# Performance work log

Measured on AMD Instinct MI355X. Metric: run time of the kernel, lower is better.

Reference implementation:

```python
import jax, jax.numpy as jnp
import numpy as np

HEAD_SIZE = 64
NUM_HEADS = 16
D_MODEL = HEAD_SIZE * NUM_HEADS  # 1024
B, S = 2, 2048


def setup_inputs() -> dict:
    key = jax.random.key(0)
    ks = jax.random.split(key, 13)
    sc = 1.0 / np.sqrt(D_MODEL)
    inp = {
        'queries': jax.random.normal(ks[0], (B, S, D_MODEL), jnp.float32),
        'keys': jax.random.normal(ks[1], (B, S, D_MODEL), jnp.float32),
        'values': jax.random.normal(ks[2], (B, S, D_MODEL), jnp.float32),
        'mask': jax.random.randint(ks[3], (B, NUM_HEADS, S, S), 0, 2, jnp.int32),
        # nn.Linear weights (out,in) and biases
        'Wq': jax.random.normal(ks[4], (D_MODEL, D_MODEL), jnp.float32) * sc,
        'bq': jax.random.normal(ks[5], (D_MODEL,), jnp.float32) * sc,
        'Wk': jax.random.normal(ks[6], (D_MODEL, D_MODEL), jnp.float32) * sc,
        'bk': jax.random.normal(ks[7], (D_MODEL,), jnp.float32) * sc,
        'Wv': jax.random.normal(ks[8], (D_MODEL, D_MODEL), jnp.float32) * sc,
        'bv': jax.random.normal(ks[9], (D_MODEL,), jnp.float32) * sc,
        'Wy': jax.random.normal(ks[10], (D_MODEL, D_MODEL), jnp.float32) * sc,
        'by': jax.random.normal(ks[11], (D_MODEL,), jnp.float32) * sc,
        # extra nn.Parameter biases (initialized to zeros in the module)
        'bq2': jnp.zeros((D_MODEL,), jnp.float32),
        'bk2': jnp.zeros((D_MODEL,), jnp.float32),
        'bv2': jnp.zeros((D_MODEL,), jnp.float32),
        'by2': jnp.zeros((D_MODEL,), jnp.float32),
    }
    return inp


def _split_heads(x):
    b, s, _ = x.shape
    return x.reshape(b, s, NUM_HEADS, HEAD_SIZE).transpose(0, 2, 1, 3)  # [B,H,S,D]


def _merge_heads(x):
    b, h, s, d = x.shape
    return x.transpose(0, 2, 1, 3).reshape(b, s, h * d)


def mha(queries, keys, values, mask, Wq, bq, bq2, Wk, bk, bk2, Wv, bv, bv2, Wy, by, by2):
    q = queries @ Wq.T + bq + bq2
    k = keys @ Wk.T + bk + bk2
    v = values @ Wv.T + bv + bv2
    q, k, v = _split_heads(q), _split_heads(k), _split_heads(v)  # [B,H,S,D]
    scores = jnp.einsum('bhqd,bhkd->bhqk', q, k) / np.sqrt(HEAD_SIZE).astype(np.float32)
    m = mask.astype(scores.dtype)
    scores = scores * m - 1e4 * (1.0 - m)
    w = jax.nn.softmax(scores, axis=-1)
    out = jnp.einsum('bhqk,bhkd->bhqd', w, v)
    y = _merge_heads(out)  # [B,S,H*D]
    return y @ Wy.T + by + by2


def reference(queries, keys, values, mask, Wq, bq, Wk, bk, Wv, bv, Wy, by, bq2, bk2, bv2, by2):
    return mha(queries, keys, values, mask, Wq, bq, bq2, Wk, bk, bk2, Wv, bv, bv2, Wy, by, by2)
```

## Files before the change

### kernel.cpp

```cpp
#include <hip/hip_runtime.h>
#include <math.h>


typedef _Float16 h8 __attribute__((ext_vector_type(8)));
typedef _Float16 h4 __attribute__((ext_vector_type(4)));
typedef float f4 __attribute__((ext_vector_type(4)));

#define S_LEN 2048
#define DM 1024
#define NH 16
#define HD 64

__global__ __launch_bounds__(256, 2) void qkv_proj_kernel(
    const float* __restrict__ Xq, const float* __restrict__ Xk, const float* __restrict__ Xv,
    const float* __restrict__ Wq, const float* __restrict__ Wk, const float* __restrict__ Wv,
    const float* __restrict__ bq, const float* __restrict__ bk, const float* __restrict__ bv,
    const float* __restrict__ bq2, const float* __restrict__ bk2, const float* __restrict__ bv2,
    _Float16* __restrict__ oq, _Float16* __restrict__ okk, _Float16* __restrict__ ov)
{
    const int z = blockIdx.z;
    const float* X  = (z == 0) ? Xq  : (z == 1) ? Xk  : Xv;
    const float* W  = (z == 0) ? Wq  : (z == 1) ? Wk  : Wv;
    const float* b1 = (z == 0) ? bq  : (z == 1) ? bk  : bv;
    const float* b2 = (z == 0) ? bq2 : (z == 1) ? bk2 : bv2;
    _Float16* outp  = (z == 0) ? oq  : (z == 1) ? okk : ov;

    __shared__ _Float16 As[128][56];
    __shared__ _Float16 Bs[128][56];

    const int tid  = threadIdx.x;
    const int lane = tid & 63;
    const int wave = tid >> 6;
    const int l16  = lane & 15;
    const int g    = lane >> 4;
    const int wm   = (wave >> 1) * 64;
    const int wn   = (wave & 1) * 64;
    const int m0   = blockIdx.x * 128;
    const int n0   = blockIdx.y * 128;

    f4 acc[4][4] = {};

    for (int k0 = 0; k0 < 1024; k0 += 32) {
        __syncthreads();
        #pragma unroll
        for (int r = 0; r < 4; ++r) {
            int f = tid + 256 * r;
            int row = f >> 3;
            int c4  = (f & 7) * 4;
            f4 xa = *(const f4*)(X + (size_t)(m0 + row) * 1024 + k0 + c4);
            f4 xb = *(const f4*)(W + (size_t)(n0 + row) * 1024 + k0 + c4);
            As[row][c4 + 0] = (_Float16)xa.x; As[row][c4 + 1] = (_Float16)xa.y;
            As[row][c4 + 2] = (_Float16)xa.z; As[row][c4 + 3] = (_Float16)xa.w;
            Bs[row][c4 + 0] = (_Float16)xb.x; Bs[row][c4 + 1] = (_Float16)xb.y;
            Bs[row][c4 + 2] = (_Float16)xb.z; Bs[row][c4 + 3] = (_Float16)xb.w;
        }
        __syncthreads();

        h8 af[4], bf[4];
        #pragma unroll
        for (int i = 0; i < 4; ++i) af[i] = *(const h8*)&As[wm + i * 16 + l16][g * 8];
        #pragma unroll
        for (int j = 0; j < 4; ++j) bf[j] = *(const h8*)&Bs[wn + j * 16 + l16][g * 8];
        #pragma unroll
        for (int i = 0; i < 4; ++i)
            #pragma unroll
            for (int j = 0; j < 4; ++j)
                acc[i][j] = __builtin_amdgcn_mfma_f32_16x16x32_f16(af[i], bf[j], acc[i][j], 0, 0, 0);
    }

    #pragma unroll
    for (int i = 0; i < 4; ++i)
        #pragma unroll
        for (int j = 0; j < 4; ++j)
            #pragma unroll
            for (int r = 0; r < 4; ++r) {
                int gm = m0 + wm + i * 16 + g * 4 + r;
                int gn = n0 + wn + j * 16 + l16;
                float val = acc[i][j][r] + b1[gn] + b2[gn];
                int b = gm >> 11, s = gm & 2047;
                int h = gn >> 6,  d = gn & 63;
                outp[(((size_t)(b * NH + h) * S_LEN + s) << 6) + d] = (_Float16)val;
            }
}

__global__ __launch_bounds__(256) void transpose_v_kernel(
    const _Float16* __restrict__ v, _Float16* __restrict__ vt)
{
    const int bh = blockIdx.x;
    const int s0 = blockIdx.y * 64;
    __shared__ _Float16 t[64][65];
    const int tid = threadIdx.x;

    #pragma unroll
    for (int r = 0; r < 2; ++r) {
        int u = tid + 256 * r;
        int row = u >> 3, c8 = (u & 7) * 8;
        h8 hv = *(const h8*)(v + ((size_t)bh * S_LEN + s0 + row) * 64 + c8);
        #pragma unroll
        for (int e = 0; e < 8; ++e) t[row][c8 + e] = hv[e];
    }
    __syncthreads();
    #pragma unroll
    for (int r = 0; r < 2; ++r) {
        int u = tid + 256 * r;
        int d = u >> 3, p8 = (u & 7) * 8;
        h8 hv;
        #pragma unroll
        for (int e = 0; e < 8; ++e) {
            int p = p8 + e;
            int c = (p & 3) * 16 + (p >> 2);
            hv[e] = t[c][d];
        }
        *(h8*)(vt + ((size_t)bh * 64 + d) * S_LEN + s0 + p8) = hv;
    }
}

__global__ __launch_bounds__(256, 2) void attn_kernel(
    const _Float16* __restrict__ q_ws, const _Float16* __restrict__ k_ws,
    const _Float16* __restrict__ vt_ws, const int* __restrict__ mask,
    _Float16* __restrict__ o_ws)
{
    const int tid  = threadIdx.x;
    const int lane = tid & 63;
    const int wave = tid >> 6;
    const int g    = lane >> 4;
    const int l16  = lane & 15;
    const int qt   = blockIdx.x;
    const int bh   = blockIdx.y;
    const int q0   = qt * 128;

    __shared__ _Float16 Ks[64][72];
    __shared__ _Float16 Vs[64][72];
    __shared__ _Float16 Ps[128][72];
    __shared__ unsigned int Ms[4][128];

    h8 qf[2][2];
    #pragma unroll
    for (int i = 0; i < 2; ++i)
        #pragma unroll
        for (int ks = 0; ks < 2; ++ks)
            qf[i][ks] = *(const h8*)(q_ws +
                ((size_t)bh * S_LEN + q0 + wave * 32 + i * 16 + l16) * 64 + ks * 32 + g * 8);

    f4 oacc[2][4] = {};
    float lsum[2][4] = {};

    const int* mbase = mask + ((size_t)bh * S_LEN + q0 + wave * 32) * S_LEN;
    const int mrow = lane >> 4;

    int4 mv[8];
    #pragma unroll
    for (int c = 0; c < 8; ++c) {
        int chunk = 64 * c + lane;
        mv[c] = *(const int4*)(mbase + (size_t)(chunk >> 4) * S_LEN + (chunk & 15) * 4);
    }
    (void)mrow;

    for (int kt = 0; kt < 32; ++kt) {
        const int k0 = kt * 64;
        const int kn = ((kt + 1) & 31) * 64;

        __syncthreads();
        #pragma unroll
        for (int r = 0; r < 2; ++r) {
            int u = tid + 256 * r;
            int row = u >> 3, c8 = (u & 7) * 8;
            *(h8*)&Ks[row][c8] = *(const h8*)(k_ws + ((size_t)bh * S_LEN + k0 + row) * 64 + c8);
            *(h8*)&Vs[row][c8] = *(const h8*)(vt_ws + ((size_t)bh * 64 + row) * S_LEN + k0 + c8);
        }
        __syncthreads();

        f4 sacc[2][4] = {};
        #pragma unroll
        for (int ks = 0; ks < 2; ++ks) {
            h8 kf[4];
            #pragma unroll
            for (int j = 0; j < 4; ++j) kf[j] = *(const h8*)&Ks[j * 16 + l16][ks * 32 + g * 8];
            #pragma unroll
            for (int i = 0; i < 2; ++i)
                #pragma unroll
                for (int j = 0; j < 4; ++j)
                    sacc[i][j] = __builtin_amdgcn_mfma_f32_16x16x32_f16(qf[i][ks], kf[j], sacc[i][j], 0, 0, 0);
        }

        #pragma unroll
        for (int c = 0; c < 8; ++c) {
            int chunk = 64 * c + lane;
            unsigned nib = (unsigned)(mv[c].x != 0)
                         | ((unsigned)(mv[c].y != 0) << 1)
                         | ((unsigned)(mv[c].z != 0) << 2)
                         | ((unsigned)(mv[c].w != 0) << 3);
            int rr = chunk >> 4, c4 = chunk & 15;
            ((unsigned char*)&Ms[wave][0])[rr * 16 + (c4 & 3) * 4 + (c4 >> 2)] =
                (unsigned char)nib;
        }
        #pragma unroll
        for (int c = 0; c < 8; ++c) {
            int chunk = 64 * c + lane;
            mv[c] = *(const int4*)(mbase + (size_t)(chunk >> 4) * S_LEN + kn + (chunk & 15) * 4);
        }

        #pragma unroll
        for (int i = 0; i < 2; ++i)
            #pragma unroll
            for (int r = 0; r < 4; ++r) {
                int row_local = i * 16 + g * 4 + r;
                unsigned word = Ms[wave][row_local * 4 + (l16 >> 2)];
                unsigned sh = l16 & 3;
                float p0 = ((word >> (sh))      & 1u) ? __expf(fmaf(sacc[i][0][r], 0.125f, -5.0f)) : 0.0f;
                float p1 = ((word >> (8 + sh))  & 1u) ? __expf(fmaf(sacc[i][1][r], 0.125f, -5.0f)) : 0.0f;
                float p2 = ((word >> (16 + sh)) & 1u) ? __expf(fmaf(sacc[i][2][r], 0.125f, -5.0f)) : 0.0f;
                float p3 = ((word >> (24 + sh)) & 1u) ? __expf(fmaf(sacc[i][3][r], 0.125f, -5.0f)) : 0.0f;
                lsum[i][r] += (p0 + p1) + (p2 + p3);
                h4 ph = { (_Float16)p0, (_Float16)p1, (_Float16)p2, (_Float16)p3 };
                *(h4*)&Ps[wave * 32 + i * 16 + g * 4 + r][l16 * 4] = ph;
            }

        #pragma unroll
        for (int ks = 0; ks < 2; ++ks) {
            h8 pf[2], vf[4];
            #pragma unroll
            for (int i = 0; i < 2; ++i)  pf[i]  = *(const h8*)&Ps[wave * 32 + i * 16 + l16][ks * 32 + g * 8];
            #pragma unroll
            for (int jd = 0; jd < 4; ++jd) vf[jd] = *(const h8*)&Vs[jd * 16 + l16][ks * 32 + g * 8];
            #pragma unroll
            for (int i = 0; i < 2; ++i)
                #pragma unroll
                for (int jd = 0; jd < 4; ++jd)
                    oacc[i][jd] = __builtin_amdgcn_mfma_f32_16x16x32_f16(pf[i], vf[jd], oacc[i][jd], 0, 0, 0);
        }
    }

    const int b = bh >> 4, h = bh & 15;
    #pragma unroll
    for (int i = 0; i < 2; ++i)
        #pragma unroll
        for (int r = 0; r < 4; ++r) {
            float l = lsum[i][r];
            l += __shfl_xor(l, 1);
            l += __shfl_xor(l, 2);
            l += __shfl_xor(l, 4);
            l += __shfl_xor(l, 8);
            float inv = 1.0f / l;
            int row = q0 + wave * 32 + i * 16 + g * 4 + r;
            #pragma unroll
            for (int jd = 0; jd < 4; ++jd) {
                int d = jd * 16 + l16;
                o_ws[((size_t)b * S_LEN + row) * DM + h * 64 + d] = (_Float16)(oacc[i][jd][r] * inv);
            }
        }
}

__global__ __launch_bounds__(256, 2) void out_proj_kernel(
    const _Float16* __restrict__ A, const float* __restrict__ W,
    const float* __restrict__ b1, const float* __restrict__ b2,
    float* __restrict__ out)
{
    __shared__ _Float16 As[128][56];
    __shared__ _Float16 Bs[128][56];

    const int tid  = threadIdx.x;
    const int lane = tid & 63;
    const int wave = tid >> 6;
    const int l16  = lane & 15;
    const int g    = lane >> 4;
    const int wm   = (wave >> 1) * 64;
    const int wn   = (wave & 1) * 64;
    const int m0   = blockIdx.x * 128;
    const int n0   = blockIdx.y * 128;

    f4 acc[4][4] = {};

    for (int k0 = 0; k0 < 1024; k0 += 32) {
        __syncthreads();
        #pragma unroll
        for (int r = 0; r < 2; ++r) {
            int u = tid + 256 * r;
            int row = u >> 2, c8 = (u & 3) * 8;
            *(h8*)&As[row][c8] = *(const h8*)(A + (size_t)(m0 + row) * 1024 + k0 + c8);
        }
        #pragma unroll
        for (int r = 0; r < 4; ++r) {
            int f = tid + 256 * r;
            int row = f >> 3, c4 = (f & 7) * 4;
            f4 xb = *(const f4*)(W + (size_t)(n0 + row) * 1024 + k0 + c4);
            Bs[row][c4 + 0] = (_Float16)xb.x; Bs[row][c4 + 1] = (_Float16)xb.y;
            Bs[row][c4 + 2] = (_Float16)xb.z; Bs[row][c4 + 3] = (_Float16)xb.w;
        }
        __syncthreads();

        h8 af[4], bf[4];
        #pragma unroll
        for (int i = 0; i < 4; ++i) af[i] = *(const h8*)&As[wm + i * 16 + l16][g * 8];
        #pragma unroll
        for (int j = 0; j < 4; ++j) bf[j] = *(const h8*)&Bs[wn + j * 16 + l16][g * 8];
        #pragma unroll
        for (int i = 0; i < 4; ++i)
            #pragma unroll
            for (int j = 0; j < 4; ++j)
                acc[i][j] = __builtin_amdgcn_mfma_f32_16x16x32_f16(af[i], bf[j], acc[i][j], 0, 0, 0);
    }

    #pragma unroll
    for (int i = 0; i < 4; ++i)
        #pragma unroll
        for (int j = 0; j < 4; ++j)
            #pragma unroll
            for (int r = 0; r < 4; ++r) {
                int gm = m0 + wm + i * 16 + g * 4 + r;
                int gn = n0 + wn + j * 16 + l16;
                out[(size_t)gm * 1024 + gn] = acc[i][j][r] + b1[gn] + b2[gn];
            }
}

extern "C" void kernel_launch(void* const* d_in, const int* in_sizes, int n_in,
                              void* d_out, int out_size, void* d_ws, size_t ws_size,
                              hipStream_t stream)
{
    (void)in_sizes; (void)n_in; (void)out_size; (void)ws_size;
    const float* queries = (const float*)d_in[0];
    const float* keys    = (const float*)d_in[1];
    const float* values  = (const float*)d_in[2];
    const int*   mask    = (const int*)d_in[3];
    const float* Wq  = (const float*)d_in[4];
    const float* bq  = (const float*)d_in[5];
    const float* Wk  = (const float*)d_in[6];
    const float* bk  = (const float*)d_in[7];
    const float* Wv  = (const float*)d_in[8];
    const float* bv  = (const float*)d_in[9];
    const float* Wy  = (const float*)d_in[10];
    const float* by  = (const float*)d_in[11];
    const float* bq2 = (const float*)d_in[12];
    const float* bk2 = (const float*)d_in[13];
    const float* bv2 = (const float*)d_in[14];
    const float* by2 = (const float*)d_in[15];
    float* out = (float*)d_out;

    char* ws = (char*)d_ws;
    const size_t MB8 = (size_t)8 * 1024 * 1024;
    _Float16* q_ws  = (_Float16*)(ws);
    _Float16* k_ws  = (_Float16*)(ws + 1 * MB8);
    _Float16* v_ws  = (_Float16*)(ws + 2 * MB8);
    _Float16* vt_ws = (_Float16*)(ws + 3 * MB8);
    _Float16* o_ws  = (_Float16*)(ws + 4 * MB8);

    qkv_proj_kernel<<<dim3(32, 8, 3), 256, 0, stream>>>(
        queries, keys, values, Wq, Wk, Wv, bq, bk, bv, bq2, bk2, bv2,
        q_ws, k_ws, v_ws);
    transpose_v_kernel<<<dim3(32, 32), 256, 0, stream>>>(v_ws, vt_ws);
    attn_kernel<<<dim3(16, 32), 256, 0, stream>>>(q_ws, k_ws, vt_ws, mask, o_ws);
    out_proj_kernel<<<dim3(32, 8), 256, 0, stream>>>(o_ws, Wy, by, by2, out);
}
```

Measured before the change: 876.6 us.

## Double-buffer K, V and mask tiles in attention kernel LDS

The attention loop now keeps two LDS buffers for the K, V and packed-mask tiles. Global loads for the next tile are issued at the top of each iteration, and the data is written into the other buffer after the PV MFMAs. This cuts the two barriers per iteration to one and hides global-load latency behind compute. In exchange it uses more LDS (about 37KB per block) and more registers for the in-flight tile, which may lower occupancy at the requested 2 blocks per CU.

Result: no change. 868.2 us (-1.0%).

```diff
diff --git a/kernel.cpp b/kernel.cpp
--- a/kernel.cpp
+++ b/kernel.cpp
@@ -129,10 +129,10 @@
     const int bh   = blockIdx.y;
     const int q0   = qt * 128;
 
-    __shared__ _Float16 Ks[64][72];
-    __shared__ _Float16 Vs[64][72];
+    __shared__ _Float16 Ks[2][64][72];
+    __shared__ _Float16 Vs[2][64][72];
     __shared__ _Float16 Ps[128][72];
-    __shared__ unsigned int Ms[4][128];
+    __shared__ unsigned int Ms[2][4][128];
 
     h8 qf[2][2];
     #pragma unroll
@@ -145,37 +145,74 @@
     f4 oacc[2][4] = {};
     float lsum[2][4] = {};
 
+    const _Float16* kbase = k_ws + (size_t)bh * S_LEN * 64;
+    const _Float16* vbase = vt_ws + (size_t)bh * 64 * S_LEN;
     const int* mbase = mask + ((size_t)bh * S_LEN + q0 + wave * 32) * S_LEN;
-    const int mrow = lane >> 4;
-
-    int4 mv[8];
-    #pragma unroll
-    for (int c = 0; c < 8; ++c) {
-        int chunk = 64 * c + lane;
-        mv[c] = *(const int4*)(mbase + (size_t)(chunk >> 4) * S_LEN + (chunk & 15) * 4);
-    }
-    (void)mrow;
+
+    const int srow = tid >> 3;
+    const int sc8  = (tid & 7) * 8;
+
+    {
+        h8 k0r[2], v0r[2];
+        #pragma unroll
+        for (int r = 0; r < 2; ++r) {
+            int row = srow + 32 * r;
+            k0r[r] = *(const h8*)(kbase + (size_t)row * 64 + sc8);
+            v0r[r] = *(const h8*)(vbase + (size_t)row * S_LEN + sc8);
+        }
+        int4 m0r[8];
+        #pragma unroll
+        for (int c = 0; c < 8; ++c) {
+            int chunk = 64 * c + lane;
+            m0r[c] = *(const int4*)(mbase + (size_t)(chunk >> 4) * S_LEN + (chunk & 15) * 4);
+        }
+        #pragma unroll
+        for (int r = 0; r < 2; ++r) {
+            int row = srow + 32 * r;
+            *(h8*)&Ks[0][row][sc8] = k0r[r];
+            *(h8*)&Vs[0][row][sc8] = v0r[r];
+        }
+        #pragma unroll
+        for (int c = 0; c < 8; ++c) {
+            int chunk = 64 * c + lane;
+            unsigned nib = (unsigned)(m0r[c].x != 0)
+                         | ((unsigned)(m0r[c].y != 0) << 1)
+                         | ((unsigned)(m0r[c].z != 0) << 2)
+                         | ((unsigned)(m0r[c].w != 0) << 3);
+            int rr = chunk >> 4, c4 = chunk & 15;
+            ((unsigned char*)&Ms[0][wave][0])[rr * 16 + (c4 & 3) * 4 + (c4 >> 2)] =
+                (unsigned char)nib;
+        }
+    }
+    __syncthreads();
 
     for (int kt = 0; kt < 32; ++kt) {
-        const int k0 = kt * 64;
-        const int kn = ((kt + 1) & 31) * 64;
-
-        __syncthreads();
-        #pragma unroll
-        for (int r = 0; r < 2; ++r) {
-            int u = tid + 256 * r;
-            int row = u >> 3, c8 = (u & 7) * 8;
-            *(h8*)&Ks[row][c8] = *(const h8*)(k_ws + ((size_t)bh * S_LEN + k0 + row) * 64 + c8);
-            *(h8*)&Vs[row][c8] = *(const h8*)(vt_ws + ((size_t)bh * 64 + row) * S_LEN + k0 + c8);
-        }
-        __syncthreads();
+        const int cur = kt & 1;
+        const int nxt = cur ^ 1;
+
+        h8 knr[2], vnr[2];
+        int4 mnr[8];
+        if (kt < 31) {
+            const int k1 = (kt + 1) * 64;
+            #pragma unroll
+            for (int r = 0; r < 2; ++r) {
+                int row = srow + 32 * r;
+                knr[r] = *(const h8*)(kbase + (size_t)(k1 + row) * 64 + sc8);
+                vnr[r] = *(const h8*)(vbase + (size_t)row * S_LEN + k1 + sc8);
+            }
+            #pragma unroll
+            for (int c = 0; c < 8; ++c) {
+                int chunk = 64 * c + lane;
+                mnr[c] = *(const int4*)(mbase + (size_t)(chunk >> 4) * S_LEN + k1 + (chunk & 15) * 4);
+            }
+        }
 
         f4 sacc[2][4] = {};
         #pragma unroll
         for (int ks = 0; ks < 2; ++ks) {
             h8 kf[4];
             #pragma unroll
-            for (int j = 0; j < 4; ++j) kf[j] = *(const h8*)&Ks[j * 16 + l16][ks * 32 + g * 8];
+            for (int j = 0; j < 4; ++j) kf[j] = *(const h8*)&Ks[cur][j * 16 + l16][ks * 32 + g * 8];
             #pragma unroll
             for (int i = 0; i < 2; ++i)
                 #pragma unroll
@@ -184,28 +221,11 @@
         }
 
         #pragma unroll
-        for (int c = 0; c < 8; ++c) {
-            int chunk = 64 * c + lane;
-            unsigned nib = (unsigned)(mv[c].x != 0)
-                         | ((unsigned)(mv[c].y != 0) << 1)
-                         | ((unsigned)(mv[c].z != 0) << 2)
-                         | ((unsigned)(mv[c].w != 0) << 3);
-            int rr = chunk >> 4, c4 = chunk & 15;
-            ((unsigned char*)&Ms[wave][0])[rr * 16 + (c4 & 3) * 4 + (c4 >> 2)] =
-                (unsigned char)nib;
-        }
-        #pragma unroll
-        for (int c = 0; c < 8; ++c) {
-            int chunk = 64 * c + lane;
-            mv[c] = *(const int4*)(mbase + (size_t)(chunk >> 4) * S_LEN + kn + (chunk & 15) * 4);
-        }
-
-        #pragma unroll
         for (int i = 0; i < 2; ++i)
             #pragma unroll
             for (int r = 0; r < 4; ++r) {
                 int row_local = i * 16 + g * 4 + r;
-                unsigned word = Ms[wave][row_local * 4 + (l16 >> 2)];
+                unsigned word = Ms[cur][wave][row_local * 4 + (l16 >> 2)];
                 unsigned sh = l16 & 3;
                 float p0 = ((word >> (sh))      & 1u) ? __expf(fmaf(sacc[i][0][r], 0.125f, -5.0f)) : 0.0f;
                 float p1 = ((word >> (8 + sh))  & 1u) ? __expf(fmaf(sacc[i][1][r], 0.125f, -5.0f)) : 0.0f;
@@ -222,13 +242,34 @@
             #pragma unroll
             for (int i = 0; i < 2; ++i)  pf[i]  = *(const h8*)&Ps[wave * 32 + i * 16 + l16][ks * 32 + g * 8];
             #pragma unroll
-            for (int jd = 0; jd < 4; ++jd) vf[jd] = *(const h8*)&Vs[jd * 16 + l16][ks * 32 + g * 8];
+            for (int jd = 0; jd < 4; ++jd) vf[jd] = *(const h8*)&Vs[cur][jd * 16 + l16][ks * 32 + g * 8];
             #pragma unroll
             for (int i = 0; i < 2; ++i)
                 #pragma unroll
                 for (int jd = 0; jd < 4; ++jd)
                     oacc[i][jd] = __builtin_amdgcn_mfma_f32_16x16x32_f16(pf[i], vf[jd], oacc[i][jd], 0, 0, 0);
         }
+
+        if (kt < 31) {
+            #pragma unroll
+            for (int r = 0; r < 2; ++r) {
+                int row = srow + 32 * r;
+                *(h8*)&Ks[nxt][row][sc8] = knr[r];
+                *(h8*)&Vs[nxt][row][sc8] = vnr[r];
+            }
+            #pragma unroll
+            for (int c = 0; c < 8; ++c) {
+                int chunk = 64 * c + lane;
+                unsigned nib = (unsigned)(mnr[c].x != 0)
+                             | ((unsigned)(mnr[c].y != 0) << 1)
+                             | ((unsigned)(mnr[c].z != 0) << 2)
+                             | ((unsigned)(mnr[c].w != 0) << 3);
+                int rr = chunk >> 4, c4 = chunk & 15;
+                ((unsigned char*)&Ms[nxt][wave][0])[rr * 16 + (c4 & 3) * 4 + (c4 >> 2)] =
+                    (unsigned char)nib;
+            }
+        }
+        __syncthreads();
     }
 
     const int b = bh >> 4, h = bh & 15;
```
